# Optimization experiments

Hardware: AMD Instinct MI355X
Metric: run time of the kernel (lower is better)

Reference implementation:

```python
import jax, jax.numpy as jnp
import numpy as np

BN_EPS = 1e-5


def setup_inputs() -> dict:
    key = jax.random.key(0)
    ks = jax.random.split(key, 6)
    b, c_out, c_high = 8, 256, 512
    h1 = w1 = 64
    h2 = w2 = 32
    return {
        "fms_low": jax.random.normal(ks[0], (b, c_out, h1, w1), jnp.float32),
        "fms_high": jax.random.normal(ks[1], (b, c_high, h2, w2), jnp.float32),
        "w_conv": jax.random.normal(ks[2], (c_out, c_high), jnp.float32) * (1.0 / np.sqrt(c_high)),
        "bn_gamma": jnp.ones((c_out,), jnp.float32),
        "bn_beta": jnp.zeros((c_out,), jnp.float32),
        "bn_mean": jnp.zeros((c_out,), jnp.float32),
        "bn_var": jnp.ones((c_out,), jnp.float32),
        "fc1_w": jax.random.normal(ks[3], (c_out // 4, c_out), jnp.float32) * (1.0 / np.sqrt(c_out)),
        "fc1_b": jnp.zeros((c_out // 4,), jnp.float32),
        "fc2_w": jax.random.normal(ks[4], (c_out // 4, c_out), jnp.float32) * (1.0 / np.sqrt(c_out)),
        "fc2_b": jnp.zeros((c_out // 4,), jnp.float32),
        "scale": jax.random.normal(ks[5], (1,), jnp.float32),
    }


def reference(fms_low, fms_high, w_conv, bn_gamma, bn_beta, bn_mean, bn_var,
              fc1_w, fc1_b, fc2_w, fc2_b, scale):
    b, c, h1, w1 = fms_low.shape
    # conv_high: 1x1 conv (no bias) + BN (inference) + ReLU
    x = jnp.einsum('bchw,oc->bohw', fms_high, w_conv)  # [b, 256, h2, w2]
    inv = bn_gamma / jnp.sqrt(bn_var + BN_EPS)
    x = x * inv[None, :, None, None] + (bn_beta - bn_mean * inv)[None, :, None, None]
    x = jax.nn.relu(x)
    # raw row-major reshapes, matching torch .view(b, -1, C)
    feat_low = fms_low.reshape(b, -1, c)    # [b, N_low, 256]
    feat_high = x.reshape(b, -1, c)         # [b, N_high, 256]
    mid_low = feat_low @ fc1_w.T + fc1_b    # [b, N_low, 64]
    mid_high = feat_high @ fc2_w.T + fc2_b  # [b, N_high, 64]
    energy = jnp.einsum('bnd,bmd->bnm', mid_low, mid_high)  # [b, N_low, N_high]
    attn = jax.nn.softmax(energy, axis=-1)
    # bmm(feat_high^T, attn^T) -> [b, 256, N_low]
    mid = jnp.einsum('bmc,bnm->bcn', feat_high, attn).reshape(b, c, h1, w1)
    return scale[0] * mid
```

## Files before the change

### kernel.cpp

```cpp
#include <hip/hip_runtime.h>
#include <hip/hip_bf16.h>

typedef __bf16 v8bf __attribute__((ext_vector_type(8)));
typedef float  v4f  __attribute__((ext_vector_type(4)));

typedef __attribute__((address_space(3))) void       lds_vd;
typedef __attribute__((address_space(1))) const void gbl_vd;

#define MFMA16(a, b, c) __builtin_amdgcn_mfma_f32_16x16x32_bf16(a, b, c, 0, 0, 0)

__device__ __forceinline__ void split_hl(float v, __bf16* h, __bf16* l) {
    __bf16 hh = (__bf16)v;
    *h = hh;
    *l = (__bf16)(v - (float)hh);
}

__device__ __forceinline__ int swz_idx(int row, int col) {
    return row * 64 + ((((col >> 3) ^ (row & 7))) << 3) + (col & 7);
}
__device__ __forceinline__ const __bf16* frag_ptr(const __bf16* base, int row, int g) {
    return base + row * 64 + ((g ^ (row & 7)) << 3);
}


__global__ __launch_bounds__(256) void k_conv(
    const float* __restrict__ FH, const float* __restrict__ W,
    const float* __restrict__ gamma, const float* __restrict__ beta,
    const float* __restrict__ mean, const float* __restrict__ var,
    __bf16* __restrict__ Xhi, __bf16* __restrict__ Xlo, __bf16* __restrict__ VT)
{
    __shared__ __align__(16) __bf16 Ah[64 * 64];
    __shared__ __align__(16) __bf16 Al[64 * 64];
    __shared__ __align__(16) __bf16 Bh[64 * 64];
    __shared__ __align__(16) __bf16 Bl[64 * 64];
    __shared__ float invl[64], shl[64];

    const int tid = threadIdx.x, lane = tid & 63, w = tid >> 6;
    const int l15 = lane & 15, quad = lane >> 4;
    const int u0 = blockIdx.x * 16, o0 = blockIdx.y * 64, b = blockIdx.z;
    const float* FHb = FH + (size_t)b * 524288;

    if (tid < 64) {
        const int o = o0 + tid;
        const float iv = gamma[o] * rsqrtf(var[o] + 1e-5f);
        invl[tid] = iv;
        shl[tid] = beta[o] - mean[o] * iv;
    }

    const int ao = tid >> 2, aseg = tid & 3;
    float wreg[16], freg[16];
    {
        const float* wp = W + (size_t)(o0 + ao) * 512 + aseg * 16;
        #pragma unroll
        for (int q = 0; q < 4; ++q) {
            float4 f = ((const float4*)wp)[q];
            wreg[4*q] = f.x; wreg[4*q+1] = f.y; wreg[4*q+2] = f.z; wreg[4*q+3] = f.w;
        }
        const float* fp = FHb + (size_t)lane * 1024 + w * 256 + u0;
        #pragma unroll
        for (int q = 0; q < 4; ++q) {
            float4 f = ((const float4*)fp)[q];
            freg[4*q] = f.x; freg[4*q+1] = f.y; freg[4*q+2] = f.z; freg[4*q+3] = f.w;
        }
    }

    v4f acc[2][2];
    #pragma unroll
    for (int i = 0; i < 2; ++i)
        #pragma unroll
        for (int j = 0; j < 2; ++j) { v4f z = {0.f,0.f,0.f,0.f}; acc[i][j] = z; }
    const int oh = w >> 1, nh = w & 1;

    for (int ch = 0; ch < 8; ++ch) {
        if (ch) __syncthreads();
        #pragma unroll
        for (int z = 0; z < 2; ++z) {
            v8bf hv, lv;
            #pragma unroll
            for (int e = 0; e < 8; ++e) {
                __bf16 h, l; split_hl(wreg[8*z + e], &h, &l);
                hv[e] = h; lv[e] = l;
            }
            const int gi = (2*aseg + z) ^ (ao & 7);
            *(v8bf*)(Ah + ao*64 + (gi << 3)) = hv;
            *(v8bf*)(Al + ao*64 + (gi << 3)) = lv;
        }
        #pragma unroll
        for (int ul = 0; ul < 16; ++ul) {
            __bf16 h, l; split_hl(freg[ul], &h, &l);
            const int idx = (w*16 + ul)*64 + (((lane >> 3) ^ (ul & 7)) << 3) + (lane & 7);
            Bh[idx] = h; Bl[idx] = l;
        }
        __syncthreads();
        if (ch < 7) {
            const int c1 = (ch + 1) * 64;
            const float* wp = W + (size_t)(o0 + ao) * 512 + c1 + aseg * 16;
            #pragma unroll
            for (int q = 0; q < 4; ++q) {
                float4 f = ((const float4*)wp)[q];
                wreg[4*q] = f.x; wreg[4*q+1] = f.y; wreg[4*q+2] = f.z; wreg[4*q+3] = f.w;
            }
            const float* fp = FHb + (size_t)(c1 + lane) * 1024 + w * 256 + u0;
            #pragma unroll
            for (int q = 0; q < 4; ++q) {
                float4 f = ((const float4*)fp)[q];
                freg[4*q] = f.x; freg[4*q+1] = f.y; freg[4*q+2] = f.z; freg[4*q+3] = f.w;
            }
        }
        #pragma unroll
        for (int ks = 0; ks < 2; ++ks) {
            const int g = 4*ks + quad;
            v8bf a_h[2], a_l[2], b_h[2], b_l[2];
            #pragma unroll
            for (int i = 0; i < 2; ++i) {
                const int row = oh*32 + i*16 + l15;
                a_h[i] = *(const v8bf*)frag_ptr(Ah, row, g);
                a_l[i] = *(const v8bf*)frag_ptr(Al, row, g);
            }
            #pragma unroll
            for (int j = 0; j < 2; ++j) {
                const int row = nh*32 + j*16 + l15;
                b_h[j] = *(const v8bf*)frag_ptr(Bh, row, g);
                b_l[j] = *(const v8bf*)frag_ptr(Bl, row, g);
            }
            #pragma unroll
            for (int i = 0; i < 2; ++i)
                #pragma unroll
                for (int j = 0; j < 2; ++j) {
                    acc[i][j] = MFMA16(a_h[i], b_h[j], acc[i][j]);
                    acc[i][j] = MFMA16(a_h[i], b_l[j], acc[i][j]);
                    acc[i][j] = MFMA16(a_l[i], b_h[j], acc[i][j]);
                }
        }
    }
    __syncthreads();

    #pragma unroll
    for (int i = 0; i < 2; ++i)
        #pragma unroll
        for (int j = 0; j < 2; ++j)
            #pragma unroll
            for (int r = 0; r < 4; ++r) {
                const int row = oh*32 + i*16 + quad*4 + r;
                const int col = nh*32 + j*16 + l15;
                float v = acc[i][j][r] * invl[row] + shl[row];
                v = fmaxf(v, 0.f);
                __bf16 h, l; split_hl(v, &h, &l);
                const int idx = swz_idx(row, col);
                Ah[idx] = h; Al[idx] = l;
            }
    __syncthreads();
    {
        const int o = tid >> 2, pv = tid & 3;
        const size_t gbase = ((size_t)b*256 + o0 + o) * 1024 + pv*256 + u0;
        #pragma unroll
        for (int z = 0; z < 2; ++z) {
            const int gi = (2*pv + z) ^ (o & 7);
            v8bf h = *(v8bf*)(Ah + o*64 + (gi << 3));
            v8bf l = *(v8bf*)(Al + o*64 + (gi << 3));
            *(v8bf*)(Xhi + gbase + z*8) = h;
            *(v8bf*)(Xlo + gbase + z*8) = l;
        }
    }
    {
        const int ul = tid >> 4, s = tid & 15;
        __bf16 tmp[16];
        #pragma unroll
        for (int k = 0; k < 16; ++k) {
            const int m = s*16 + k;
            const int row = m >> 2;
            const int col = (m & 3)*16 + ul;
            tmp[k] = Ah[swz_idx(row, col)];
        }
        __bf16* vp = VT + ((size_t)b*256 + u0 + ul) * 1024 + 4*o0 + s*16;
        *(v8bf*)(vp)     = *(v8bf*)(tmp);
        *(v8bf*)(vp + 8) = *(v8bf*)(tmp + 8);
    }
}

__global__ __launch_bounds__(512) void k_proj(
    const float* __restrict__ Feat,
    const __bf16* __restrict__ Fhi, const __bf16* __restrict__ Flo,
    const float* __restrict__ W1, const float* __restrict__ b1,
    const float* __restrict__ W2, const float* __restrict__ b2,
    __bf16* __restrict__ O1hi, __bf16* __restrict__ O1lo,
    __bf16* __restrict__ O2hi, __bf16* __restrict__ O2lo)
{
    __shared__ __align__(16) __bf16 Bh[64 * 256];
    __shared__ __align__(16) __bf16 Bl[64 * 256];
    __shared__ __align__(16) __bf16 Eo[8][16 * 64];

    const int tid = threadIdx.x, lane = tid & 63, w = tid >> 6;
    const int l15 = lane & 15, quad = lane >> 4;
    const bool low = blockIdx.x < 256;
    const int r0 = (low ? blockIdx.x : (blockIdx.x - 256)) * 128;
    const int row = r0 + w*16 + l15;

    const float* Wfc = low ? W1 : W2;
    const float* bfc = low ? b1 : b2;
    __bf16* Ohi = low ? O1hi : O2hi;
    __bf16* Olo = low ? O1lo : O2lo;

    {
        const int n = tid >> 3, q8 = tid & 7, n7 = n & 7;
        const float* wp = Wfc + (size_t)n * 256 + q8 * 32;
        #pragma unroll
        for (int z = 0; z < 4; ++z) {
            float4 f0 = ((const float4*)wp)[2*z];
            float4 f1 = ((const float4*)wp)[2*z + 1];
            float w8[8] = {f0.x, f0.y, f0.z, f0.w, f1.x, f1.y, f1.z, f1.w};
            v8bf hv, lv;
            #pragma unroll
            for (int e = 0; e < 8; ++e) {
                __bf16 h, l; split_hl(w8[e], &h, &l);
                hv[e] = h; lv[e] = l;
            }
            const int gsw = (q8*4 + z) ^ n7;
            *(v8bf*)(Bh + n*256 + gsw*8) = hv;
            *(v8bf*)(Bl + n*256 + gsw*8) = lv;
        }
    }
    __syncthreads();

    v4f acc[4];
    #pragma unroll
    for (int j = 0; j < 4; ++j) { v4f z = {0.f,0.f,0.f,0.f}; acc[j] = z; }

    const int l7 = l15 & 7;
    const __bf16* bh_base = Bh + l15*256;
    const __bf16* bl_base = Bl + l15*256;

    if (low) {
        const float* ap = Feat + (size_t)row * 256 + quad * 8;
        float acur[8], anxt[8];
        {
            float4 f0 = ((const float4*)ap)[0];
            float4 f1 = ((const float4*)ap)[1];
            acur[0]=f0.x; acur[1]=f0.y; acur[2]=f0.z; acur[3]=f0.w;
            acur[4]=f1.x; acur[5]=f1.y; acur[6]=f1.z; acur[7]=f1.w;
        }
        #pragma unroll
        for (int kc = 0; kc < 8; ++kc) {
            if (kc < 7) {
                float4 f0 = ((const float4*)(ap + (kc+1)*32))[0];
                float4 f1 = ((const float4*)(ap + (kc+1)*32))[1];
                anxt[0]=f0.x; anxt[1]=f0.y; anxt[2]=f0.z; anxt[3]=f0.w;
                anxt[4]=f1.x; anxt[5]=f1.y; anxt[6]=f1.z; anxt[7]=f1.w;
            }
            v8bf ah, al;
            #pragma unroll
            for (int e = 0; e < 8; ++e) {
                __bf16 h, l; split_hl(acur[e], &h, &l);
                ah[e] = h; al[e] = l;
            }
            const int goff = (((kc*4 + quad) ^ l7) << 3);
            #pragma unroll
            for (int j = 0; j < 4; ++j) {
                v8bf bh = *(const v8bf*)(bh_base + j*4096 + goff);
                v8bf bl = *(const v8bf*)(bl_base + j*4096 + goff);
                acc[j] = MFMA16(ah, bh, acc[j]);
                acc[j] = MFMA16(ah, bl, acc[j]);
                acc[j] = MFMA16(al, bh, acc[j]);
            }
            #pragma unroll
            for (int e = 0; e < 8; ++e) acur[e] = anxt[e];
        }
    } else {
        const __bf16* fh = Fhi + (size_t)row * 256 + quad * 8;
        const __bf16* fl = Flo + (size_t)row * 256 + quad * 8;
        v8bf ah = *(const v8bf*)(fh);
        v8bf al = *(const v8bf*)(fl);
        #pragma unroll
        for (int kc = 0; kc < 8; ++kc) {
            v8bf anh, anl;
            if (kc < 7) {
                anh = *(const v8bf*)(fh + (kc+1)*32);
                anl = *(const v8bf*)(fl + (kc+1)*32);
            }
            const int goff = (((kc*4 + quad) ^ l7) << 3);
            #pragma unroll
            for (int j = 0; j < 4; ++j) {
                v8bf bh = *(const v8bf*)(bh_base + j*4096 + goff);
                v8bf bl = *(const v8bf*)(bl_base + j*4096 + goff);
                acc[j] = MFMA16(ah, bh, acc[j]);
                acc[j] = MFMA16(ah, bl, acc[j]);
                acc[j] = MFMA16(al, bh, acc[j]);
            }
            if (kc < 7) { ah = anh; al = anl; }
        }
    }

    __bf16* eo = &Eo[w][0];
    __bf16 lb[4][4];
    #pragma unroll
    for (int j = 0; j < 4; ++j) {
        const float bias = bfc[j*16 + l15];
        #pragma unroll
        for (int r = 0; r < 4; ++r) {
            __bf16 h, l; split_hl(acc[j][r] + bias, &h, &l);
            lb[j][r] = l;
            eo[swz_idx(quad*4 + r, j*16 + l15)] = h;
        }
    }
    const size_t orow = (size_t)row * 64;
    #pragma unroll
    for (int z = 0; z < 2; ++z) {
        const int gi = (2*quad + z) ^ l7;
        *(v8bf*)(Ohi + orow + quad*16 + z*8) = *(v8bf*)(eo + l15*64 + gi*8);
    }
    #pragma unroll
    for (int j = 0; j < 4; ++j)
        #pragma unroll
        for (int r = 0; r < 4; ++r)
            eo[swz_idx(quad*4 + r, j*16 + l15)] = lb[j][r];
    #pragma unroll
    for (int z = 0; z < 2; ++z) {
        const int gi = (2*quad + z) ^ l7;
        *(v8bf*)(Olo + orow + quad*16 + z*8) = *(v8bf*)(eo + l15*64 + gi*8);
    }
}

__global__ __launch_bounds__(512, 4) void k_attn(
    const __bf16* __restrict__ MLhi, const __bf16* __restrict__ MLlo,
    const __bf16* __restrict__ MHhi, const __bf16* __restrict__ MHlo,
    const __bf16* __restrict__ VT,
    const float* __restrict__ scale_p,
    float* __restrict__ out)
{
    __shared__ __align__(16) __bf16 Khi[3][32 * 64];
    __shared__ __align__(16) __bf16 Klo[3][32 * 64];
    __shared__ __align__(16) __bf16 Vs [2][256 * 32];
    __shared__ __align__(16) __bf16 Ps [2][4][16 * 32];
    __shared__ float lsh[2][4][16];

    const int tid = threadIdx.x, lane = tid & 63, w = tid >> 6;
    const int l15 = lane & 15, quad = lane >> 4;
    const int b = blockIdx.x & 7, qtb = blockIdx.x >> 3;
    const int q0 = qtb * 64;
    const int qt = w & 3, mb = w >> 2;

    v8bf qhi[2], qlo[2];
    {
        const __bf16* qp  = MLhi + ((size_t)(b*4096 + q0 + qt*16 + l15)) * 64;
        const __bf16* qlp = MLlo + ((size_t)(b*4096 + q0 + qt*16 + l15)) * 64;
        #pragma unroll
        for (int h = 0; h < 2; ++h) {
            qhi[h] = *(const v8bf*)(qp + h*32 + quad*8);
            qlo[h] = *(const v8bf*)(qlp + h*32 + quad*8);
        }
    }
    #pragma unroll
    for (int h = 0; h < 2; ++h) {
        asm volatile("" : "+v"(qhi[h]));
        asm volatile("" : "+v"(qlo[h]));
    }

    const char* Khg = (const char*)(MHhi + (size_t)b * 65536);
    const char* Klg = (const char*)(MHlo + (size_t)b * 65536);
    const char* Vg  = (const char*)(VT + (size_t)b * 262144);
    const int offK = (lane >> 3) * 128 + (((lane & 7) ^ ((lane >> 3) & 7)) << 4);
    const int offV = (lane >> 2) * 2048 + ((((lane & 3) ^ ((lane >> 3) & 3))) << 4);

    const char* kgsrc = (w < 4) ? Khg : Klg;
    const int ksub = (w & 3) * 1024;
    char* kdst_base = (char*)((w < 4) ? &Khi[0][0] : &Klo[0][0]);

    v4f oacc[4][2];
    #pragma unroll
    for (int t = 0; t < 4; ++t)
        #pragma unroll
        for (int cb = 0; cb < 2; ++cb) { v4f z = {0.f,0.f,0.f,0.f}; oacc[t][cb] = z; }
    float lrow[4] = {0.f, 0.f, 0.f, 0.f};

    {
        __builtin_amdgcn_global_load_lds((gbl_vd*)(kgsrc + ksub + offK),
                                         (lds_vd*)(kdst_base + ksub), 16, 0, 0);
        __builtin_amdgcn_global_load_lds((gbl_vd*)(kgsrc + 4096 + ksub + offK),
                                         (lds_vd*)(kdst_base + 4096 + ksub), 16, 0, 0);
        #pragma unroll
        for (int j = 0; j < 2; ++j) {
            const int i = w*2 + j;
            __builtin_amdgcn_global_load_lds((gbl_vd*)(Vg + i*32768 + offV),
                                             (lds_vd*)((char*)&Vs[0][0] + i*1024), 16, 0, 0);
        }
    }
    asm volatile("s_waitcnt vmcnt(3)\n\ts_barrier" ::: "memory");

    int kb = 0;
    for (int ch = 0; ch < 32; ++ch) {
        const int cur = ch & 1, nxt = cur ^ 1;
        const int mn  = ((ch < 31) ? (ch + 1) : 31) * 32;
        const int mn2 = ((ch < 30) ? (ch + 2) : 31) * 32;
        const int sd  = (kb >= 1) ? (kb - 1) : 2;

        __builtin_amdgcn_global_load_lds((gbl_vd*)(kgsrc + mn2*128 + ksub + offK),
                                         (lds_vd*)(kdst_base + sd*4096 + ksub), 16, 0, 0);

        v4f s0 = {0.f, 0.f, 0.f, 0.f}, s1 = {0.f, 0.f, 0.f, 0.f};
        __builtin_amdgcn_s_setprio(1);
        {
            const int row = mb*16 + l15;
            v8bf kh0 = *(const v8bf*)frag_ptr(&Khi[kb][0], row, quad);
            v8bf kl0 = *(const v8bf*)frag_ptr(&Klo[kb][0], row, quad);
            v8bf kh1 = *(const v8bf*)frag_ptr(&Khi[kb][0], row, 4 + quad);
            v8bf kl1 = *(const v8bf*)frag_ptr(&Klo[kb][0], row, 4 + quad);
            s0 = MFMA16(qhi[0], kh0, s0);
            s1 = MFMA16(qhi[1], kh1, s1);
            s0 = MFMA16(qhi[0], kl0, s0);
            s1 = MFMA16(qhi[1], kl1, s1);
            s0 = MFMA16(qlo[0], kh0, s0);
            s1 = MFMA16(qlo[1], kh1, s1);
        }
        __builtin_amdgcn_s_setprio(0);
        v4f sacc = s0 + s1;

        #pragma unroll
        for (int r = 0; r < 4; ++r) {
            const float p = __expf(sacc[r]);
            lrow[r] += p;
            const int row = quad*4 + r;
            const int slot = (mb*2 + (l15 >> 3)) ^ ((row >> 1) & 3);
            Ps[cur][qt][row*32 + (slot << 3) + (l15 & 7)] = (__bf16)p;
        }

        if (ch) {
            const int pb = nxt;
            v8bf pa[4];
            #pragma unroll
            for (int t = 0; t < 4; ++t)
                pa[t] = *(const v8bf*)(&Ps[pb][t][0] + l15*32 + ((quad ^ ((l15 >> 1) & 3)) << 3));
            __builtin_amdgcn_s_setprio(1);
            #pragma unroll
            for (int cb = 0; cb < 2; ++cb) {
                const int vrow = w*32 + cb*16 + l15;
                v8bf vv = *(const v8bf*)(&Vs[pb][0] + vrow*32 + ((quad ^ ((vrow >> 1) & 3)) << 3));
                #pragma unroll
                for (int t = 0; t < 4; ++t)
                    oacc[t][cb] = MFMA16(pa[t], vv, oacc[t][cb]);
            }
            __builtin_amdgcn_s_setprio(0);
        }

        asm volatile("s_waitcnt lgkmcnt(0)" ::: "memory");
        #pragma unroll
        for (int j = 0; j < 2; ++j) {
            const int i = w*2 + j;
            __builtin_amdgcn_global_load_lds((gbl_vd*)(Vg + mn*2 + i*32768 + offV),
                                             (lds_vd*)((char*)&Vs[nxt][0] + i*1024), 16, 0, 0);
        }

        asm volatile("s_waitcnt vmcnt(3) lgkmcnt(0)\n\ts_barrier" ::: "memory");

        kb = (kb < 2) ? (kb + 1) : 0;
    }

    {
        v8bf pa[4];
        #pragma unroll
        for (int t = 0; t < 4; ++t)
            pa[t] = *(const v8bf*)(&Ps[1][t][0] + l15*32 + ((quad ^ ((l15 >> 1) & 3)) << 3));
        #pragma unroll
        for (int cb = 0; cb < 2; ++cb) {
            const int vrow = w*32 + cb*16 + l15;
            v8bf vv = *(const v8bf*)(&Vs[1][0] + vrow*32 + ((quad ^ ((vrow >> 1) & 3)) << 3));
            #pragma unroll
            for (int t = 0; t < 4; ++t)
                oacc[t][cb] = MFMA16(pa[t], vv, oacc[t][cb]);
        }
    }

    #pragma unroll
    for (int r = 0; r < 4; ++r) {
        float s = lrow[r];
        #pragma unroll
        for (int d = 1; d < 16; d <<= 1) s += __shfl_xor(s, d, 64);
        lrow[r] = s;
    }
    if (l15 == 0) {
        #pragma unroll
        for (int r = 0; r < 4; ++r) lsh[mb][qt][quad*4 + r] = lrow[r];
    }
    __syncthreads();

    const float scl = scale_p[0];
    float inv[4][4];
    #pragma unroll
    for (int t = 0; t < 4; ++t)
        #pragma unroll
        for (int r = 0; r < 4; ++r)
            inv[t][r] = scl / (lsh[0][t][quad*4 + r] + lsh[1][t][quad*4 + r]);
    float* outb = out + (size_t)b * 256 * 4096;
    #pragma unroll
    for (int cb = 0; cb < 2; ++cb) {
        const int c = w*32 + cb*16 + l15;
        #pragma unroll
        for (int t = 0; t < 4; ++t) {
            float4 v;
            v.x = oacc[t][cb][0] * inv[t][0];
            v.y = oacc[t][cb][1] * inv[t][1];
            v.z = oacc[t][cb][2] * inv[t][2];
            v.w = oacc[t][cb][3] * inv[t][3];
            *(float4*)(outb + (size_t)c * 4096 + q0 + t*16 + quad*4) = v;
        }
    }
}

extern "C" void kernel_launch(void* const* d_in, const int* in_sizes, int n_in,
                              void* d_out, int out_size, void* d_ws, size_t ws_size,
                              hipStream_t stream)
{
    const float* fms_low  = (const float*)d_in[0];
    const float* fms_high = (const float*)d_in[1];
    const float* w_conv   = (const float*)d_in[2];
    const float* gamma    = (const float*)d_in[3];
    const float* beta     = (const float*)d_in[4];
    const float* mean     = (const float*)d_in[5];
    const float* var      = (const float*)d_in[6];
    const float* fc1_w    = (const float*)d_in[7];
    const float* fc1_b    = (const float*)d_in[8];
    const float* fc2_w    = (const float*)d_in[9];
    const float* fc2_b    = (const float*)d_in[10];
    const float* scale    = (const float*)d_in[11];
    float* out = (float*)d_out;

    __bf16* Xhi  = (__bf16*)d_ws;
    __bf16* Xlo  = Xhi  + (size_t)8*256*1024;
    __bf16* VT   = Xlo  + (size_t)8*256*1024;
    __bf16* MLhi = VT   + (size_t)8*256*1024;
    __bf16* MLlo = MLhi + (size_t)8*4096*64;
    __bf16* MHhi = MLlo + (size_t)8*4096*64;
    __bf16* MHlo = MHhi + (size_t)8*1024*64;

    k_conv<<<dim3(16, 4, 8), 256, 0, stream>>>(fms_high, w_conv, gamma, beta,
                                               mean, var, Xhi, Xlo, VT);
    k_proj<<<dim3(320), 512, 0, stream>>>(fms_low, Xhi, Xlo,
                                          fc1_w, fc1_b, fc2_w, fc2_b,
                                          MLhi, MLlo, MHhi, MHlo);
    k_attn<<<dim3(512), 512, 0, stream>>>(MLhi, MLlo, MHhi, MHlo, VT, scale, out);
}
```

Baseline: 176.4 us.

## Load V fragments directly into registers instead of staging through LDS

Removes the shared-memory V double buffer and its global_load_lds staging. Each wave now loads its own V fragments straight from global memory into registers, one chunk ahead. The loop is unrolled by two so the A/B register sets alternate without dynamic indexing. This cuts LDS traffic and capacity, which may allow higher occupancy, but it exposes global-load latency directly to the MFMA consumers. The vmcnt accounting also now mixes K LDS-loads with V register loads.

```diff
diff --git a/kernel.cpp b/kernel.cpp
--- a/kernel.cpp
+++ b/kernel.cpp
@@ -329,7 +329,6 @@
 {
     __shared__ __align__(16) __bf16 Khi[3][32 * 64];
     __shared__ __align__(16) __bf16 Klo[3][32 * 64];
-    __shared__ __align__(16) __bf16 Vs [2][256 * 32];
     __shared__ __align__(16) __bf16 Ps [2][4][16 * 32];
     __shared__ float lsh[2][4][16];
 
@@ -357,14 +356,15 @@
 
     const char* Khg = (const char*)(MHhi + (size_t)b * 65536);
     const char* Klg = (const char*)(MHlo + (size_t)b * 65536);
-    const char* Vg  = (const char*)(VT + (size_t)b * 262144);
     const int offK = (lane >> 3) * 128 + (((lane & 7) ^ ((lane >> 3) & 7)) << 4);
-    const int offV = (lane >> 2) * 2048 + ((((lane & 3) ^ ((lane >> 3) & 3))) << 4);
 
     const char* kgsrc = (w < 4) ? Khg : Klg;
     const int ksub = (w & 3) * 1024;
     char* kdst_base = (char*)((w < 4) ? &Khi[0][0] : &Klo[0][0]);
 
+    const __bf16* vp0 = VT + (size_t)b * 262144 + (size_t)(w*32 + l15)      * 1024 + quad*8;
+    const __bf16* vp1 = VT + (size_t)b * 262144 + (size_t)(w*32 + 16 + l15) * 1024 + quad*8;
+
     v4f oacc[4][2];
     #pragma unroll
     for (int t = 0; t < 4; ++t)
@@ -372,86 +372,90 @@
         for (int cb = 0; cb < 2; ++cb) { v4f z = {0.f,0.f,0.f,0.f}; oacc[t][cb] = z; }
     float lrow[4] = {0.f, 0.f, 0.f, 0.f};
 
-    {
-        __builtin_amdgcn_global_load_lds((gbl_vd*)(kgsrc + ksub + offK),
-                                         (lds_vd*)(kdst_base + ksub), 16, 0, 0);
-        __builtin_amdgcn_global_load_lds((gbl_vd*)(kgsrc + 4096 + ksub + offK),
-                                         (lds_vd*)(kdst_base + 4096 + ksub), 16, 0, 0);
-        #pragma unroll
-        for (int j = 0; j < 2; ++j) {
-            const int i = w*2 + j;
-            __builtin_amdgcn_global_load_lds((gbl_vd*)(Vg + i*32768 + offV),
-                                             (lds_vd*)((char*)&Vs[0][0] + i*1024), 16, 0, 0);
-        }
-    }
-    asm volatile("s_waitcnt vmcnt(3)\n\ts_barrier" ::: "memory");
-
+    __builtin_amdgcn_global_load_lds((gbl_vd*)(kgsrc + ksub + offK),
+                                     (lds_vd*)(kdst_base + ksub), 16, 0, 0);
+    __builtin_amdgcn_global_load_lds((gbl_vd*)(kgsrc + 4096 + ksub + offK),
+                                     (lds_vd*)(kdst_base + 4096 + ksub), 16, 0, 0);
+    asm volatile("s_waitcnt vmcnt(1)\n\ts_barrier" ::: "memory");
+
+    v8bf vA0, vA1, vB0, vB1;
     int kb = 0;
-    for (int ch = 0; ch < 32; ++ch) {
-        const int cur = ch & 1, nxt = cur ^ 1;
-        const int mn  = ((ch < 31) ? (ch + 1) : 31) * 32;
-        const int mn2 = ((ch < 30) ? (ch + 2) : 31) * 32;
-        const int sd  = (kb >= 1) ? (kb - 1) : 2;
-
-        __builtin_amdgcn_global_load_lds((gbl_vd*)(kgsrc + mn2*128 + ksub + offK),
-                                         (lds_vd*)(kdst_base + sd*4096 + ksub), 16, 0, 0);
-
-        v4f s0 = {0.f, 0.f, 0.f, 0.f}, s1 = {0.f, 0.f, 0.f, 0.f};
-        __builtin_amdgcn_s_setprio(1);
+
+    #define QK_BODY(KBUF, PAR)                                                  \
+    {                                                                           \
+        v4f s0 = {0.f,0.f,0.f,0.f}, s1 = {0.f,0.f,0.f,0.f};                     \
+        __builtin_amdgcn_s_setprio(1);                                          \
+        const int row = mb*16 + l15;                                            \
+        v8bf kh0 = *(const v8bf*)frag_ptr(&Khi[KBUF][0], row, quad);            \
+        v8bf kl0 = *(const v8bf*)frag_ptr(&Klo[KBUF][0], row, quad);            \
+        v8bf kh1 = *(const v8bf*)frag_ptr(&Khi[KBUF][0], row, 4 + quad);        \
+        v8bf kl1 = *(const v8bf*)frag_ptr(&Klo[KBUF][0], row, 4 + quad);        \
+        s0 = MFMA16(qhi[0], kh0, s0);                                           \
+        s1 = MFMA16(qhi[1], kh1, s1);                                           \
+        s0 = MFMA16(qhi[0], kl0, s0);                                           \
+        s1 = MFMA16(qhi[1], kl1, s1);                                           \
+        s0 = MFMA16(qlo[0], kh0, s0);                                           \
+        s1 = MFMA16(qlo[1], kh1, s1);                                           \
+        __builtin_amdgcn_s_setprio(0);                                          \
+        v4f sacc = s0 + s1;                                                     \
+        _Pragma("unroll")                                                       \
+        for (int r = 0; r < 4; ++r) {                                           \
+            const float p = __expf(sacc[r]);                                    \
+            lrow[r] += p;                                                       \
+            const int prow = quad*4 + r;                                        \
+            const int slot = (mb*2 + (l15 >> 3)) ^ ((prow >> 1) & 3);           \
+            Ps[PAR][qt][prow*32 + (slot << 3) + (l15 & 7)] = (__bf16)p;         \
+        }                                                                       \
+    }
+
+    #define PV_BODY(PAR, V0, V1)                                                \
+    {                                                                           \
+        v8bf pa[4];                                                             \
+        _Pragma("unroll")                                                       \
+        for (int t = 0; t < 4; ++t)                                             \
+            pa[t] = *(const v8bf*)(&Ps[PAR][t][0] + l15*32 +                    \
+                                   ((quad ^ ((l15 >> 1) & 3)) << 3));           \
+        __builtin_amdgcn_s_setprio(1);                                          \
+        _Pragma("unroll")                                                       \
+        for (int t = 0; t < 4; ++t) {                                           \
+            oacc[t][0] = MFMA16(pa[t], V0, oacc[t][0]);                         \
+            oacc[t][1] = MFMA16(pa[t], V1, oacc[t][1]);                         \
+        }                                                                       \
+        __builtin_amdgcn_s_setprio(0);                                          \
+    }
+
+    for (int it = 0; it < 16; ++it) {
+        const int ch0 = 2*it, ch1 = 2*it + 1;
+
         {
-            const int row = mb*16 + l15;
-            v8bf kh0 = *(const v8bf*)frag_ptr(&Khi[kb][0], row, quad);
-            v8bf kl0 = *(const v8bf*)frag_ptr(&Klo[kb][0], row, quad);
-            v8bf kh1 = *(const v8bf*)frag_ptr(&Khi[kb][0], row, 4 + quad);
-            v8bf kl1 = *(const v8bf*)frag_ptr(&Klo[kb][0], row, 4 + quad);
-            s0 = MFMA16(qhi[0], kh0, s0);
-            s1 = MFMA16(qhi[1], kh1, s1);
-            s0 = MFMA16(qhi[0], kl0, s0);
-            s1 = MFMA16(qhi[1], kl1, s1);
-            s0 = MFMA16(qlo[0], kh0, s0);
-            s1 = MFMA16(qlo[1], kh1, s1);
-        }
-        __builtin_amdgcn_s_setprio(0);
-        v4f sacc = s0 + s1;
-
-        #pragma unroll
-        for (int r = 0; r < 4; ++r) {
-            const float p = __expf(sacc[r]);
-            lrow[r] += p;
-            const int row = quad*4 + r;
-            const int slot = (mb*2 + (l15 >> 3)) ^ ((row >> 1) & 3);
-            Ps[cur][qt][row*32 + (slot << 3) + (l15 & 7)] = (__bf16)p;
-        }
-
-        if (ch) {
-            const int pb = nxt;
-            v8bf pa[4];
-            #pragma unroll
-            for (int t = 0; t < 4; ++t)
-                pa[t] = *(const v8bf*)(&Ps[pb][t][0] + l15*32 + ((quad ^ ((l15 >> 1) & 3)) << 3));
-            __builtin_amdgcn_s_setprio(1);
-            #pragma unroll
-            for (int cb = 0; cb < 2; ++cb) {
-                const int vrow = w*32 + cb*16 + l15;
-                v8bf vv = *(const v8bf*)(&Vs[pb][0] + vrow*32 + ((quad ^ ((vrow >> 1) & 3)) << 3));
-                #pragma unroll
-                for (int t = 0; t < 4; ++t)
-                    oacc[t][cb] = MFMA16(pa[t], vv, oacc[t][cb]);
-            }
-            __builtin_amdgcn_s_setprio(0);
-        }
-
-        asm volatile("s_waitcnt lgkmcnt(0)" ::: "memory");
-        #pragma unroll
-        for (int j = 0; j < 2; ++j) {
-            const int i = w*2 + j;
-            __builtin_amdgcn_global_load_lds((gbl_vd*)(Vg + mn*2 + i*32768 + offV),
-                                             (lds_vd*)((char*)&Vs[nxt][0] + i*1024), 16, 0, 0);
-        }
-
-        asm volatile("s_waitcnt vmcnt(3) lgkmcnt(0)\n\ts_barrier" ::: "memory");
-
-        kb = (kb < 2) ? (kb + 1) : 0;
+            const int mn2 = ((ch0 < 30) ? (ch0 + 2) : 31) * 32;
+            const int sd  = (kb >= 1) ? (kb - 1) : 2;
+            __builtin_amdgcn_global_load_lds((gbl_vd*)(kgsrc + mn2*128 + ksub + offK),
+                                             (lds_vd*)(kdst_base + sd*4096 + ksub), 16, 0, 0);
+            vA0 = *(const v8bf*)(vp0 + ch0*32);
+            vA1 = *(const v8bf*)(vp1 + ch0*32);
+
+            QK_BODY(kb, 0)
+            if (it) PV_BODY(1, vB0, vB1)
+
+            asm volatile("s_waitcnt vmcnt(3) lgkmcnt(0)\n\ts_barrier" ::: "memory");
+            kb = (kb < 2) ? (kb + 1) : 0;
+        }
+
+        {
+            const int mn2 = ((ch1 < 30) ? (ch1 + 2) : 31) * 32;
+            const int sd  = (kb >= 1) ? (kb - 1) : 2;
+            __builtin_amdgcn_global_load_lds((gbl_vd*)(kgsrc + mn2*128 + ksub + offK),
+                                             (lds_vd*)(kdst_base + sd*4096 + ksub), 16, 0, 0);
+            vB0 = *(const v8bf*)(vp0 + ch1*32);
+            vB1 = *(const v8bf*)(vp1 + ch1*32);
+
+            QK_BODY(kb, 1)
+            PV_BODY(0, vA0, vA1)
+
+            asm volatile("s_waitcnt vmcnt(3) lgkmcnt(0)\n\ts_barrier" ::: "memory");
+            kb = (kb < 2) ? (kb + 1) : 0;
+        }
     }
 
     {
@@ -460,14 +464,13 @@
         for (int t = 0; t < 4; ++t)
             pa[t] = *(const v8bf*)(&Ps[1][t][0] + l15*32 + ((quad ^ ((l15 >> 1) & 3)) << 3));
         #pragma unroll
-        for (int cb = 0; cb < 2; ++cb) {
-            const int vrow = w*32 + cb*16 + l15;
-            v8bf vv = *(const v8bf*)(&Vs[1][0] + vrow*32 + ((quad ^ ((vrow >> 1) & 3)) << 3));
-            #pragma unroll
-            for (int t = 0; t < 4; ++t)
-                oacc[t][cb] = MFMA16(pa[t], vv, oacc[t][cb]);
-        }
-    }
+        for (int t = 0; t < 4; ++t) {
+            oacc[t][0] = MFMA16(pa[t], vB0, oacc[t][0]);
+            oacc[t][1] = MFMA16(pa[t], vB1, oacc[t][1]);
+        }
+    }
+    #undef QK_BODY
+    #undef PV_BODY
 
     #pragma unroll
     for (int r = 0; r < 4; ++r) {
```

Measured after the change: 182.9 us. 1.04x slower.
